# Kernel tuning notes

Hardware: AMD Instinct MI355X
Metric: run time of the kernel (lower is better)

The kernel has to match this reference:

```python
import jax, jax.numpy as jnp
import numpy as np

L, E, D, R = 3, 4, 1024, 64   # num_layer, num_expert, embed_dim, low_rank
B = 16384                     # batch


def _xavier(key, shape, fan_in, fan_out):
    lim = np.sqrt(6.0 / (fan_in + fan_out)).astype(np.float32)
    return jax.random.uniform(key, shape, jnp.float32, -lim, lim)


def setup_inputs() -> dict:
    key = jax.random.key(0)
    ks = jax.random.split(key, 5)
    x = jax.random.normal(ks[0], (B, D), jnp.float32)
    U = _xavier(ks[1], (L, E, D, R), D, R)   # per-layer per-expert U: D x r
    V = _xavier(ks[2], (L, E, R, D), R, D)   # per-layer per-expert V: r x D
    C = _xavier(ks[3], (L, E, R, R), R, R)   # per-layer per-expert C: r x r
    Wg = _xavier(ks[4], (L, E, D), D, 1)     # gating weights (one Linear(D,1) per expert)
    b = jnp.zeros((L, D), jnp.float32)       # per-layer bias
    return {"x": x, "U": U, "V": V, "C": C, "Wg": Wg, "b": b}


def _cross_layer(xl, U, V, C, Wg, b):
    # xl: [B,D]; U: [E,D,R]; V: [E,R,D]; C: [E,R,R]; Wg: [E,D]; b: [D]
    v = jnp.tanh(jnp.einsum('erd,bd->ber', V, xl))          # [B,E,R]
    c = jnp.tanh(jnp.einsum('ers,bes->ber', C, v))          # [B,E,R]
    u = jnp.einsum('edr,ber->bed', U, c) + b                # [B,E,D]
    g = jax.nn.softmax(jnp.einsum('ed,bd->be', Wg, xl), axis=-1)  # [B,E]
    return jnp.einsum('be,bed->bd', g, u)                   # [B,D]


def reference(x, U, V, C, Wg, b):
    x0 = x
    xl = x
    for i in range(L - 1):
        xl = jnp.tanh(_cross_layer(xl, U[i], V[i], C[i], Wg[i], b[i]) * x0 + xl)
    xl = _cross_layer(xl, U[L - 1], V[L - 1], C[L - 1], Wg[L - 1], b[L - 1]) * x0 + xl
    return xl
```

## Files before the change

kernel.cpp:

```cpp
#include <hip/hip_runtime.h>
#include <hip/hip_bf16.h>


typedef _Float16 f16;
typedef f16  f16x4v __attribute__((ext_vector_type(4)));
typedef f16  f16x8 __attribute__((ext_vector_type(8)));
typedef float f32x4 __attribute__((ext_vector_type(4)));

#define B_TOT 16384
#define DDIM  1024
#define RLOW  64
#define NEXP  4
#define NLAY  3
#define BT    64

__device__ __forceinline__ float ftanh(float x) {
    float e2 = __expf(2.0f * x);
    return 1.0f - 2.0f / (e2 + 1.0f);
}
__device__ __forceinline__ f32x4 mfma16(f16x8 a, f16x8 b, f32x4 c) {
    return __builtin_amdgcn_mfma_f32_16x16x32_f16(a, b, c, 0, 0, 0);
}
__device__ __forceinline__ int xl_off(int row, int col) {
    return row * 2048 + ((col * 2) ^ ((row & 7) << 4));
}
__device__ __forceinline__ int sv_off(int row, int col) {
    return row * 512 + ((col * 2) ^ ((row & 7) << 4));
}

__global__ void cast_f32_to_f16(const float* __restrict__ in,
                                f16* __restrict__ out, int n4) {
    int i = blockIdx.x * 256 + threadIdx.x;
    if (i < n4) {
        float4 v = reinterpret_cast<const float4*>(in)[i];
        f16 h0 = (f16)v.x, h1 = (f16)v.y, h2 = (f16)v.z, h3 = (f16)v.w;
        short4 pk;
        pk.x = __builtin_bit_cast(short, h0); pk.y = __builtin_bit_cast(short, h1);
        pk.z = __builtin_bit_cast(short, h2); pk.w = __builtin_bit_cast(short, h3);
        reinterpret_cast<short4*>(out)[i] = pk;
    }
}

__global__ void build_wgh(const float* __restrict__ Wg, f16* __restrict__ Wgh) {
    int i = blockIdx.x * 256 + threadIdx.x;
    int l = i >> 14, r = (i >> 10) & 15, k = i & 1023;
    f16 v = (f16)0.f;
    if (r < NEXP) v = (f16)Wg[(size_t)(l * NEXP + r) * DDIM + k];
    Wgh[i] = v;
}

__global__ __launch_bounds__(512, 1) void crossnet_fused(
    const float* __restrict__ x, float* __restrict__ out,
    const f16* __restrict__ Uh,
    const f16* __restrict__ Vh,
    const f16* __restrict__ Ch,
    const f16* __restrict__ Wgh,
    const float* __restrict__ bias)
{
    __shared__ f16 s_xl[BT * 1024];
    __shared__ f16 s_v[BT * 256];

    const int tid  = threadIdx.x;
    const int lane = tid & 63;
    const int wv   = tid >> 6;
    const int l16  = lane & 15;
    const int lhi  = lane >> 4;
    const int row0 = blockIdx.x * BT;
    const int eown = wv >> 1;
    const int hown = wv & 1;

#pragma unroll
    for (int j = 0; j < 16; ++j) {
        int f = tid + j * 512;
        int row = f >> 7, seg = f & 127;
        const float4* sp = reinterpret_cast<const float4*>(
            x + (size_t)(row0 + row) * DDIM + seg * 8);
        float4 a = sp[0], b = sp[1];
        f16x8 h;
        h[0]=(f16)a.x; h[1]=(f16)a.y; h[2]=(f16)a.z; h[3]=(f16)a.w;
        h[4]=(f16)b.x; h[5]=(f16)b.y; h[6]=(f16)b.z; h[7]=(f16)b.w;
        *reinterpret_cast<f16x8*>((char*)s_xl + xl_off(row, seg * 8)) = h;
    }

#pragma unroll 1
    for (int l = 0; l < NLAY; ++l) {
        const f16* Vl = Vh  + (size_t)l * 256 * DDIM;
        const f16* Ul = Uh  + (size_t)l * NEXP * DDIM * RLOW;
        const f16* Cl = Ch  + (size_t)l * NEXP * RLOW * RLOW;
        const f16* Wl = Wgh + (size_t)l * 16 * DDIM;
        const float* bl = bias + (size_t)l * DDIM;
        const int last = (l == NLAY - 1);

        __syncthreads();

        const f16* B0 = Vl + (size_t)(2 * wv * 16 + l16) * DDIM + lhi * 8;
        const f16* B1 = Vl + (size_t)((2 * wv + 1) * 16 + l16) * DDIM + lhi * 8;
        const f16* BG = Wl + (size_t)l16 * DDIM + lhi * 8;
        f32x4 a0[4], a1[4], ag[4];
#pragma unroll
        for (int mt = 0; mt < 4; ++mt) {
            a0[mt] = (f32x4){0.f,0.f,0.f,0.f};
            a1[mt] = (f32x4){0.f,0.f,0.f,0.f};
            ag[mt] = (f32x4){0.f,0.f,0.f,0.f};
        }
#pragma unroll 4
        for (int kt = 0; kt < 32; ++kt) {
            f16x8 b0 = *reinterpret_cast<const f16x8*>(B0 + kt * 32);
            f16x8 b1 = *reinterpret_cast<const f16x8*>(B1 + kt * 32);
            f16x8 bg = *reinterpret_cast<const f16x8*>(BG + kt * 32);
#pragma unroll
            for (int mt = 0; mt < 4; ++mt) {
                f16x8 af = *reinterpret_cast<const f16x8*>(
                    (char*)s_xl + xl_off(mt * 16 + l16, kt * 32 + lhi * 8));
                a0[mt] = mfma16(b0, af, a0[mt]);
                a1[mt] = mfma16(b1, af, a1[mt]);
                ag[mt] = mfma16(bg, af, ag[mt]);
            }
        }

        float gmy[4];
#pragma unroll
        for (int mt = 0; mt < 4; ++mt) {
            float e0 = ag[mt][0], e1 = ag[mt][1], e2 = ag[mt][2], e3 = ag[mt][3];
            float mx = fmaxf(fmaxf(e0, e1), fmaxf(e2, e3));
            float x0e = __expf(e0 - mx), x1e = __expf(e1 - mx);
            float x2e = __expf(e2 - mx), x3e = __expf(e3 - mx);
            float inv = 1.0f / (x0e + x1e + x2e + x3e);
            float ge = (eown == 0) ? x0e : (eown == 1) ? x1e : (eown == 2) ? x2e : x3e;
            gmy[mt] = __shfl(ge * inv, l16);
        }

#pragma unroll
        for (int mt = 0; mt < 4; ++mt) {
            const int m = mt * 16 + l16;
            f16x4v w0, w1;
#pragma unroll
            for (int r = 0; r < 4; ++r) {
                w0[r] = (f16)ftanh(a0[mt][r]);
                w1[r] = (f16)ftanh(a1[mt][r]);
            }
            *reinterpret_cast<f16x4v*>((char*)s_v + sv_off(m, (2 * wv) * 16 + lhi * 4))     = w0;
            *reinterpret_cast<f16x4v*>((char*)s_v + sv_off(m, (2 * wv + 1) * 16 + lhi * 4)) = w1;
        }

        __syncthreads();

        f16x8 caf[4][2];
#pragma unroll
        for (int mt = 0; mt < 4; ++mt)
#pragma unroll
            for (int kt2 = 0; kt2 < 2; ++kt2)
                caf[mt][kt2] = *reinterpret_cast<const f16x8*>(
                    (char*)s_v + sv_off(mt * 16 + l16, eown * 64 + kt2 * 32 + lhi * 8));

        __syncthreads();

        {
            f32x4 c2[4][2];
#pragma unroll
            for (int mt = 0; mt < 4; ++mt) {
                c2[mt][0] = (f32x4){0.f,0.f,0.f,0.f};
                c2[mt][1] = (f32x4){0.f,0.f,0.f,0.f};
            }
            const f16* CB0 = Cl + (size_t)(eown * 64 + hown * 32 + l16) * RLOW + lhi * 8;
            const f16* CB1 = CB0 + 16 * RLOW;
#pragma unroll
            for (int kt2 = 0; kt2 < 2; ++kt2) {
                f16x8 cb0 = *reinterpret_cast<const f16x8*>(CB0 + kt2 * 32);
                f16x8 cb1 = *reinterpret_cast<const f16x8*>(CB1 + kt2 * 32);
#pragma unroll
                for (int mt = 0; mt < 4; ++mt) {
                    c2[mt][0] = mfma16(cb0, caf[mt][kt2], c2[mt][0]);
                    c2[mt][1] = mfma16(cb1, caf[mt][kt2], c2[mt][1]);
                }
            }
#pragma unroll
            for (int mt = 0; mt < 4; ++mt) {
                const int m = mt * 16 + l16;
#pragma unroll
                for (int ntc = 0; ntc < 2; ++ntc) {
                    f16x4v w;
#pragma unroll
                    for (int r = 0; r < 4; ++r)
                        w[r] = (f16)(ftanh(c2[mt][ntc][r]) * gmy[mt]);
                    const int col = eown * 64 + hown * 32 + ntc * 16 + lhi * 4;
                    *reinterpret_cast<f16x4v*>((char*)s_v + sv_off(m, col)) = w;
                }
            }
        }

        __syncthreads();

#pragma unroll 1
        for (int ps = 0; ps < 2; ++ps) {
            const int dbase = wv * 128 + ps * 64;
            f32x4 c3[4][4];
#pragma unroll
            for (int dt = 0; dt < 4; ++dt)
#pragma unroll
                for (int mt = 0; mt < 4; ++mt) c3[dt][mt] = (f32x4){0.f,0.f,0.f,0.f};
#pragma unroll 4
            for (int kt = 0; kt < 8; ++kt) {
                const size_t ebase = (size_t)(kt >> 1) * DDIM * RLOW + (kt & 1) * 32 + lhi * 8;
                f16x8 af[4];
#pragma unroll
                for (int mt = 0; mt < 4; ++mt)
                    af[mt] = *reinterpret_cast<const f16x8*>(
                        (char*)s_v + sv_off(mt * 16 + l16, kt * 32 + lhi * 8));
#pragma unroll
                for (int dt = 0; dt < 4; ++dt) {
                    const f16* ub = Ul + ebase + (size_t)(dbase + dt * 16 + l16) * RLOW;
                    f16x8 bf = *reinterpret_cast<const f16x8*>(ub);
#pragma unroll
                    for (int mt = 0; mt < 4; ++mt)
                        c3[dt][mt] = mfma16(bf, af[mt], c3[dt][mt]);
                }
            }
            f32x4 biasv[4];
#pragma unroll
            for (int dt = 0; dt < 4; ++dt)
                biasv[dt] = *reinterpret_cast<const f32x4*>(bl + dbase + dt * 16 + lhi * 4);
#pragma unroll
            for (int dt = 0; dt < 4; ++dt) {
                const int d0 = dbase + dt * 16 + lhi * 4;
#pragma unroll
                for (int mt = 0; mt < 4; ++mt) {
                    const int m = mt * 16 + l16;
                    f32x4 x0v = *reinterpret_cast<const f32x4*>(
                        x + (size_t)(row0 + m) * DDIM + d0);
                    f32x4 xlv;
                    if (l == 0) {
                        xlv = x0v;
                    } else {
                        f16x4v h = *reinterpret_cast<const f16x4v*>(
                            (char*)s_xl + xl_off(m, d0));
                        xlv[0] = (float)h[0]; xlv[1] = (float)h[1];
                        xlv[2] = (float)h[2]; xlv[3] = (float)h[3];
                    }
                    f32x4 y;
#pragma unroll
                    for (int r = 0; r < 4; ++r)
                        y[r] = fmaf(c3[dt][mt][r] + biasv[dt][r], x0v[r], xlv[r]);
                    if (!last) {
                        f16x4v hw;
#pragma unroll
                        for (int r = 0; r < 4; ++r) hw[r] = (f16)ftanh(y[r]);
                        *reinterpret_cast<f16x4v*>((char*)s_xl + xl_off(m, d0)) = hw;
                    } else {
                        __builtin_nontemporal_store(y,
                            reinterpret_cast<f32x4*>(out + (size_t)(row0 + m) * DDIM + d0));
                    }
                }
            }
        }
    }
}

extern "C" void kernel_launch(void* const* d_in, const int* in_sizes, int n_in,
                              void* d_out, int out_size, void* d_ws, size_t ws_size,
                              hipStream_t stream)
{
    const float* x  = (const float*)d_in[0];
    const float* U  = (const float*)d_in[1];
    const float* V  = (const float*)d_in[2];
    const float* C  = (const float*)d_in[3];
    const float* Wg = (const float*)d_in[4];
    const float* bb = (const float*)d_in[5];
    float* out = (float*)d_out;

    const size_t sUV = (size_t)NEXP * DDIM * RLOW;
    const size_t sC  = (size_t)NEXP * RLOW * RLOW;
    const size_t sW  = (size_t)16 * DDIM;

    f16* Vh  = (f16*)d_ws;
    f16* Uh  = Vh + NLAY * sUV;
    f16* Chh = Uh + NLAY * sUV;
    f16* Wgh = Chh + NLAY * sC;

    int n4v = (int)(NLAY * sUV / 4);
    cast_f32_to_f16<<<(n4v + 255) / 256, 256, 0, stream>>>(V, Vh, n4v);
    cast_f32_to_f16<<<(n4v + 255) / 256, 256, 0, stream>>>(U, Uh, n4v);
    int n4c = (int)(NLAY * sC / 4);
    cast_f32_to_f16<<<(n4c + 255) / 256, 256, 0, stream>>>(C, Chh, n4c);
    build_wgh<<<(int)(NLAY * sW / 256), 256, 0, stream>>>(Wg, Wgh);

    crossnet_fused<<<dim3(B_TOT / BT), dim3(512), 0, stream>>>(
        x, out, Uh, Vh, Chh, Wgh, bb);
}
```

Before: 196.0 us.

## Repartition V/gate projection per expert-and-row-half to drop block barriers

Each wave now computes all 64 V-projection columns for its own expert over half of the tile's rows, instead of 32 columns over all 64 rows. Because the same wave then runs the C-stage on exactly those rows and columns, two __syncthreads between the V and C stages can be removed. The redundant gating MFMAs per wave are also halved, and fewer LDS reads of xl are needed. In exchange, each wave issues twice as many global/L2 loads of V fragments per k-step, and register pressure changes from the new accumulator shapes.

```diff
diff --git a/kernel.cpp b/kernel.cpp
--- a/kernel.cpp
+++ b/kernel.cpp
@@ -68,6 +68,10 @@
     const int row0 = blockIdx.x * BT;
     const int eown = wv >> 1;
     const int hown = wv & 1;
+    const int mbase = hown * 32;
+
+    char* const xlb = (char*)s_xl;
+    char* const svb = (char*)s_v;
 
 #pragma unroll
     for (int j = 0; j < 16; ++j) {
@@ -79,7 +83,7 @@
         f16x8 h;
         h[0]=(f16)a.x; h[1]=(f16)a.y; h[2]=(f16)a.z; h[3]=(f16)a.w;
         h[4]=(f16)b.x; h[5]=(f16)b.y; h[6]=(f16)b.z; h[7]=(f16)b.w;
-        *reinterpret_cast<f16x8*>((char*)s_xl + xl_off(row, seg * 8)) = h;
+        *reinterpret_cast<f16x8*>(xlb + xl_off(row, seg * 8)) = h;
     }
 
 #pragma unroll 1
@@ -93,34 +97,36 @@
 
         __syncthreads();
 
-        const f16* B0 = Vl + (size_t)(2 * wv * 16 + l16) * DDIM + lhi * 8;
-        const f16* B1 = Vl + (size_t)((2 * wv + 1) * 16 + l16) * DDIM + lhi * 8;
-        const f16* BG = Wl + (size_t)l16 * DDIM + lhi * 8;
-        f32x4 a0[4], a1[4], ag[4];
-#pragma unroll
-        for (int mt = 0; mt < 4; ++mt) {
-            a0[mt] = (f32x4){0.f,0.f,0.f,0.f};
-            a1[mt] = (f32x4){0.f,0.f,0.f,0.f};
-            ag[mt] = (f32x4){0.f,0.f,0.f,0.f};
-        }
+        const f16* Vb0 = Vl + (size_t)(64 * eown + l16) * DDIM + lhi * 8;
+        const f16* BG  = Wl + (size_t)l16 * DDIM + lhi * 8;
+        f32x4 a1[4][2], ag[2];
+#pragma unroll
+        for (int nt = 0; nt < 4; ++nt)
+#pragma unroll
+            for (int mt = 0; mt < 2; ++mt) a1[nt][mt] = (f32x4){0.f,0.f,0.f,0.f};
+        ag[0] = (f32x4){0.f,0.f,0.f,0.f};
+        ag[1] = (f32x4){0.f,0.f,0.f,0.f};
 #pragma unroll 4
         for (int kt = 0; kt < 32; ++kt) {
-            f16x8 b0 = *reinterpret_cast<const f16x8*>(B0 + kt * 32);
-            f16x8 b1 = *reinterpret_cast<const f16x8*>(B1 + kt * 32);
-            f16x8 bg = *reinterpret_cast<const f16x8*>(BG + kt * 32);
-#pragma unroll
-            for (int mt = 0; mt < 4; ++mt) {
+            f16x8 bv[4], bg;
+#pragma unroll
+            for (int nt = 0; nt < 4; ++nt)
+                bv[nt] = *reinterpret_cast<const f16x8*>(Vb0 + (size_t)nt * 16 * DDIM + kt * 32);
+            bg = *reinterpret_cast<const f16x8*>(BG + kt * 32);
+#pragma unroll
+            for (int mt = 0; mt < 2; ++mt) {
                 f16x8 af = *reinterpret_cast<const f16x8*>(
-                    (char*)s_xl + xl_off(mt * 16 + l16, kt * 32 + lhi * 8));
-                a0[mt] = mfma16(b0, af, a0[mt]);
-                a1[mt] = mfma16(b1, af, a1[mt]);
+                    xlb + xl_off(mbase + mt * 16 + l16, kt * 32 + lhi * 8));
+#pragma unroll
+                for (int nt = 0; nt < 4; ++nt)
+                    a1[nt][mt] = mfma16(bv[nt], af, a1[nt][mt]);
                 ag[mt] = mfma16(bg, af, ag[mt]);
             }
         }
 
-        float gmy[4];
-#pragma unroll
-        for (int mt = 0; mt < 4; ++mt) {
+        float gmy[2];
+#pragma unroll
+        for (int mt = 0; mt < 2; ++mt) {
             float e0 = ag[mt][0], e1 = ag[mt][1], e2 = ag[mt][2], e3 = ag[mt][3];
             float mx = fmaxf(fmaxf(e0, e1), fmaxf(e2, e3));
             float x0e = __expf(e0 - mx), x1e = __expf(e1 - mx);
@@ -131,60 +137,53 @@
         }
 
 #pragma unroll
-        for (int mt = 0; mt < 4; ++mt) {
-            const int m = mt * 16 + l16;
-            f16x4v w0, w1;
-#pragma unroll
-            for (int r = 0; r < 4; ++r) {
-                w0[r] = (f16)ftanh(a0[mt][r]);
-                w1[r] = (f16)ftanh(a1[mt][r]);
-            }
-            *reinterpret_cast<f16x4v*>((char*)s_v + sv_off(m, (2 * wv) * 16 + lhi * 4))     = w0;
-            *reinterpret_cast<f16x4v*>((char*)s_v + sv_off(m, (2 * wv + 1) * 16 + lhi * 4)) = w1;
-        }
-
-        __syncthreads();
-
-        f16x8 caf[4][2];
-#pragma unroll
-        for (int mt = 0; mt < 4; ++mt)
+        for (int nt = 0; nt < 4; ++nt)
+#pragma unroll
+            for (int mt = 0; mt < 2; ++mt) {
+                const int m = mbase + mt * 16 + l16;
+                f16x4v w;
+#pragma unroll
+                for (int r = 0; r < 4; ++r) w[r] = (f16)ftanh(a1[nt][mt][r]);
+                *reinterpret_cast<f16x4v*>(svb + sv_off(m, 64 * eown + nt * 16 + lhi * 4)) = w;
+            }
+
+        f16x8 caf[2][2];
+#pragma unroll
+        for (int mt = 0; mt < 2; ++mt)
 #pragma unroll
             for (int kt2 = 0; kt2 < 2; ++kt2)
                 caf[mt][kt2] = *reinterpret_cast<const f16x8*>(
-                    (char*)s_v + sv_off(mt * 16 + l16, eown * 64 + kt2 * 32 + lhi * 8));
-
-        __syncthreads();
+                    svb + sv_off(mbase + mt * 16 + l16, 64 * eown + kt2 * 32 + lhi * 8));
 
         {
-            f32x4 c2[4][2];
-#pragma unroll
-            for (int mt = 0; mt < 4; ++mt) {
-                c2[mt][0] = (f32x4){0.f,0.f,0.f,0.f};
-                c2[mt][1] = (f32x4){0.f,0.f,0.f,0.f};
-            }
-            const f16* CB0 = Cl + (size_t)(eown * 64 + hown * 32 + l16) * RLOW + lhi * 8;
-            const f16* CB1 = CB0 + 16 * RLOW;
+            f32x4 c2[2][4];
+#pragma unroll
+            for (int mt = 0; mt < 2; ++mt)
+#pragma unroll
+                for (int ct = 0; ct < 4; ++ct) c2[mt][ct] = (f32x4){0.f,0.f,0.f,0.f};
+            const f16* Cb = Cl + (size_t)(64 * eown + l16) * RLOW + lhi * 8;
 #pragma unroll
             for (int kt2 = 0; kt2 < 2; ++kt2) {
-                f16x8 cb0 = *reinterpret_cast<const f16x8*>(CB0 + kt2 * 32);
-                f16x8 cb1 = *reinterpret_cast<const f16x8*>(CB1 + kt2 * 32);
-#pragma unroll
-                for (int mt = 0; mt < 4; ++mt) {
-                    c2[mt][0] = mfma16(cb0, caf[mt][kt2], c2[mt][0]);
-                    c2[mt][1] = mfma16(cb1, caf[mt][kt2], c2[mt][1]);
-                }
-            }
-#pragma unroll
-            for (int mt = 0; mt < 4; ++mt) {
-                const int m = mt * 16 + l16;
-#pragma unroll
-                for (int ntc = 0; ntc < 2; ++ntc) {
+#pragma unroll
+                for (int ct = 0; ct < 4; ++ct) {
+                    f16x8 cb = *reinterpret_cast<const f16x8*>(
+                        Cb + (size_t)ct * 16 * RLOW + kt2 * 32);
+#pragma unroll
+                    for (int mt = 0; mt < 2; ++mt)
+                        c2[mt][ct] = mfma16(cb, caf[mt][kt2], c2[mt][ct]);
+                }
+            }
+#pragma unroll
+            for (int mt = 0; mt < 2; ++mt) {
+                const int m = mbase + mt * 16 + l16;
+#pragma unroll
+                for (int ct = 0; ct < 4; ++ct) {
                     f16x4v w;
 #pragma unroll
                     for (int r = 0; r < 4; ++r)
-                        w[r] = (f16)(ftanh(c2[mt][ntc][r]) * gmy[mt]);
-                    const int col = eown * 64 + hown * 32 + ntc * 16 + lhi * 4;
-                    *reinterpret_cast<f16x4v*>((char*)s_v + sv_off(m, col)) = w;
+                        w[r] = (f16)(ftanh(c2[mt][ct][r]) * gmy[mt]);
+                    *reinterpret_cast<f16x4v*>(
+                        svb + sv_off(m, 64 * eown + ct * 16 + lhi * 4)) = w;
                 }
             }
         }
@@ -201,15 +200,15 @@
                 for (int mt = 0; mt < 4; ++mt) c3[dt][mt] = (f32x4){0.f,0.f,0.f,0.f};
 #pragma unroll 4
             for (int kt = 0; kt < 8; ++kt) {
-                const size_t ebase = (size_t)(kt >> 1) * DDIM * RLOW + (kt & 1) * 32 + lhi * 8;
                 f16x8 af[4];
 #pragma unroll
                 for (int mt = 0; mt < 4; ++mt)
                     af[mt] = *reinterpret_cast<const f16x8*>(
-                        (char*)s_v + sv_off(mt * 16 + l16, kt * 32 + lhi * 8));
+                        svb + sv_off(mt * 16 + l16, kt * 32 + lhi * 8));
 #pragma unroll
                 for (int dt = 0; dt < 4; ++dt) {
-                    const f16* ub = Ul + ebase + (size_t)(dbase + dt * 16 + l16) * RLOW;
+                    const f16* ub = Ul + (size_t)(kt >> 1) * DDIM * RLOW
+                        + (size_t)(dbase + dt * 16 + l16) * RLOW + (kt & 1) * 32 + lhi * 8;
                     f16x8 bf = *reinterpret_cast<const f16x8*>(ub);
 #pragma unroll
                     for (int mt = 0; mt < 4; ++mt)
@@ -232,10 +231,9 @@
                     if (l == 0) {
                         xlv = x0v;
                     } else {
-                        f16x4v h = *reinterpret_cast<const f16x4v*>(
-                            (char*)s_xl + xl_off(m, d0));
-                        xlv[0] = (float)h[0]; xlv[1] = (float)h[1];
-                        xlv[2] = (float)h[2]; xlv[3] = (float)h[3];
+                        f16x4v hx = *reinterpret_cast<const f16x4v*>(xlb + xl_off(m, d0));
+                        xlv[0] = (float)hx[0]; xlv[1] = (float)hx[1];
+                        xlv[2] = (float)hx[2]; xlv[3] = (float)hx[3];
                     }
                     f32x4 y;
 #pragma unroll
@@ -245,7 +243,7 @@
                         f16x4v hw;
 #pragma unroll
                         for (int r = 0; r < 4; ++r) hw[r] = (f16)ftanh(y[r]);
-                        *reinterpret_cast<f16x4v*>((char*)s_xl + xl_off(m, d0)) = hw;
+                        *reinterpret_cast<f16x4v*>(xlb + xl_off(m, d0)) = hw;
                     } else {
                         __builtin_nontemporal_store(y,
                             reinterpret_cast<f32x4*>(out + (size_t)(row0 + m) * DDIM + d0));
```

Result: slower. 234.1 us (+19.5%).
